# Kernel optimization log

Hardware: AMD Instinct MI355X
Metric: run time of the kernel (lower is better)

The kernel has to match this reference:

```python
import jax, jax.numpy as jnp
import numpy as np

B, N, K, D, H = 32, 4096, 8, 256, 512
ITERS = 3
LN_EPS = 1e-5  # torch LayerNorm default; self.eps is unused in forward


def _ln(x, g, b):
    m = jnp.mean(x, axis=-1, keepdims=True)
    v = jnp.mean(jnp.square(x - m), axis=-1, keepdims=True)
    return (x - m) * jax.lax.rsqrt(v + LN_EPS) * g + b


def setup_inputs() -> dict:
    key = jax.random.key(0)
    ks = jax.random.split(key, 16)
    s = 0.02
    return {
        "inputs": jax.random.normal(ks[0], (B, N, D), jnp.float32),
        "slots_init": jax.random.normal(ks[1], (B, K, D), jnp.float32),
        "ln_in_g": jnp.ones((D,), jnp.float32), "ln_in_b": jnp.zeros((D,), jnp.float32),
        "ln_s_g": jnp.ones((D,), jnp.float32), "ln_s_b": jnp.zeros((D,), jnp.float32),
        "ln_ff_g": jnp.ones((D,), jnp.float32), "ln_ff_b": jnp.zeros((D,), jnp.float32),
        "Wk": s * jax.random.normal(ks[2], (D, D), jnp.float32), "bk": jnp.zeros((D,), jnp.float32),
        "Wq": s * jax.random.normal(ks[3], (D, D), jnp.float32), "bq": jnp.zeros((D,), jnp.float32),
        "Wv": s * jax.random.normal(ks[4], (D, D), jnp.float32), "bv": jnp.zeros((D,), jnp.float32),
        "W_ih": s * jax.random.normal(ks[5], (3 * D, D), jnp.float32),
        "b_ih": jnp.zeros((3 * D,), jnp.float32),
        "W_hh": s * jax.random.normal(ks[6], (3 * D, D), jnp.float32),
        "b_hh": jnp.zeros((3 * D,), jnp.float32),
        "W1": s * jax.random.normal(ks[7], (H, D), jnp.float32), "b1": jnp.zeros((H,), jnp.float32),
        "W2": s * jax.random.normal(ks[8], (D, H), jnp.float32), "b2": jnp.zeros((D,), jnp.float32),
    }


def _gru_cell(x, h, W_ih, b_ih, W_hh, b_hh):
    # PyTorch GRUCell: gates in order r, z, n
    gi = x @ W_ih.T + b_ih  # [*, 3D]
    gh = h @ W_hh.T + b_hh
    ir, iz, inn = jnp.split(gi, 3, axis=-1)
    hr, hz, hn = jnp.split(gh, 3, axis=-1)
    r = jax.nn.sigmoid(ir + hr)
    z = jax.nn.sigmoid(iz + hz)
    n = jnp.tanh(inn + r * hn)
    return (1.0 - z) * n + z * h


def reference(inputs, slots_init, ln_in_g, ln_in_b, ln_s_g, ln_s_b, ln_ff_g, ln_ff_b,
              Wk, bk, Wq, bq, Wv, bv, W_ih, b_ih, W_hh, b_hh, W1, b1, W2, b2):
    d = inputs.shape[-1]
    x = _ln(inputs, ln_in_g, ln_in_b)  # [B,N,D]
    # k, v depend only on x; hoisted out of the loop (same math as source)
    k = x @ Wk.T + bk                  # project_inputs
    v = x @ Wv.T + bv                  # project_v
    scale = 1.0 / jnp.sqrt(jnp.asarray(d, inputs.dtype))
    slots = slots_init
    for _ in range(ITERS):
        slots_prev = slots
        q = _ln(slots, ln_s_g, ln_s_b) @ Wq.T + bq          # [B,K,D]
        attn_logits = jnp.einsum('bkd,bnd->bkn', q, k) * scale
        # competitive softmax over the SLOT axis (dim=1), not keys
        attn = jax.nn.softmax(attn_logits, axis=1)          # [B,K,N]
        updates = jnp.einsum('bkn,bnd->bkd', attn, v)
        slots = _gru_cell(updates, slots_prev, W_ih, b_ih, W_hh, b_hh)
        hdd = jax.nn.relu(_ln(slots, ln_ff_g, ln_ff_b) @ W1.T + b1)
        slots = slots + hdd @ W2.T + b2
    return slots
```

## Files before the change

### kernel.cpp

```cpp
#include <hip/hip_runtime.h>
#include <hip/hip_bf16.h>
#include <cstddef>
#include <cstdint>

#define BB 32
#define NN 4096
#define KK 8
#define DD 256
#define HH 512
#define LN_EPS 1e-5f
#define SCALE 0.0625f
#define NCHUNK 32

__device__ __forceinline__ float wave_sum(float v) {
#pragma unroll
  for (int off = 32; off >= 1; off >>= 1) v += __shfl_xor(v, off);
  return v;
}

__device__ __forceinline__ float sigmoidf_(float x) { return 1.0f / (1.0f + __expf(-x)); }

__device__ __forceinline__ float bflo(uint u) { return __uint_as_float(u << 16); }
__device__ __forceinline__ float bfhi(uint u) { return __uint_as_float(u & 0xffff0000u); }

#define OFF_G   0
#define OFF_W1  393216
#define OFF_W2  524288
#define OFF_WV  655360
#define OFF_WQ  720896
#define OFF_WK  786432
#define WB_ELEMS 851968

#define G_PRE (BB * KK)
#define G_W2B (512 * 11)
#define G_SETUP (G_PRE + G_W2B + 1)

__device__ __forceinline__ float dotp4(uint2 w, float4 s) {
  return __uint_as_float(w.x << 16) * s.x + __uint_as_float(w.x & 0xffff0000u) * s.y +
         __uint_as_float(w.y << 16) * s.z + __uint_as_float(w.y & 0xffff0000u) * s.w;
}

template <int OUT, int KL>
__device__ __forceinline__ float gemv_p(const ushort* __restrict__ wt, int j, int kb,
                                        const float* __restrict__ src) {
  const uint2* p = (const uint2*)(wt + ((size_t)(kb >> 2) * OUT + j) * 4);
  float a = 0.0f;
#pragma unroll 16
  for (int e = 0; e < KL / 4; ++e) {
    uint2 w = p[(size_t)e * OUT];
    float4 s = *(const float4*)(src + kb + e * 4);
    a += dotp4(w, s);
  }
  return a;
}

__global__ __launch_bounds__(256) void k_setup(
    const float* __restrict__ Wih, const float* __restrict__ Whh,
    const float* __restrict__ W1, const float* __restrict__ W2,
    const float* __restrict__ Wv, const float* __restrict__ Wq,
    const float* __restrict__ Wk, ushort* __restrict__ wb,
    const float* __restrict__ slots, const float* __restrict__ gs, const float* __restrict__ bs,
    const float* __restrict__ bq, const float* __restrict__ bk,
    const float* __restrict__ gi, const float* __restrict__ bi,
    const float* __restrict__ bv, float* __restrict__ bvw,
    float* __restrict__ qk, float* __restrict__ qb) {
  int blk = blockIdx.x;
  if (blk < G_PRE) {
    int row = blk;
    int t = threadIdx.x;
    int wid = t >> 6, lane = t & 63;
    __shared__ float lns[DD];
    __shared__ float qs[DD];
    __shared__ float rb[8];
    float sv = slots[(size_t)row * DD + t];
    float s = wave_sum(sv);
    float s2 = wave_sum(sv * sv);
    if (lane == 0) { rb[wid] = s; rb[4 + wid] = s2; }
    __syncthreads();
    float tot = rb[0] + rb[1] + rb[2] + rb[3];
    float tot2 = rb[4] + rb[5] + rb[6] + rb[7];
    float m = tot * (1.0f / DD);
    float var = tot2 * (1.0f / DD) - m * m;
    float rs = rsqrtf(var + LN_EPS);
    lns[t] = (sv - m) * rs * gs[t] + bs[t];
    __syncthreads();
    float acc = 0.0f;
    const float4* wr = (const float4*)(Wq + (size_t)t * DD);
#pragma unroll 4
    for (int e4 = 0; e4 < DD / 4; ++e4) {
      float4 w = wr[e4];
      float4 l = ((const float4*)lns)[e4];
      acc += w.x * l.x + w.y * l.y + w.z * l.z + w.w * l.w;
    }
    qs[t] = acc + bq[t];
    __syncthreads();
    float a2 = 0.0f;
    for (int d = 0; d < DD; ++d) a2 = fmaf(qs[d], Wk[(size_t)d * DD + t], a2);
    float a2S = SCALE * a2;
    qk[(size_t)row * DD + t] = a2S * gi[t];
    float pb = wave_sum(qs[t] * bk[t]);
    float pb2 = wave_sum(a2S * bi[t]);
    __syncthreads();
    if (lane == 0) { rb[wid] = pb; rb[4 + wid] = pb2; }
    __syncthreads();
    if (t == 0) qb[row] = SCALE * (rb[0] + rb[1] + rb[2] + rb[3]) + rb[4] + rb[5] + rb[6] + rb[7];
  } else if (blk < G_PRE + G_W2B) {
    int q2 = blk - G_PRE;
    int m = q2 >> 9;
    int idx = (q2 & 511) * 256 + threadIdx.x;
    const int sizes[11] = {65536, 65536, 65536, 65536, 65536, 65536, 131072, 131072, 65536, 65536, 65536};
    const int offs[11] = {OFF_G, OFF_G + 65536, OFF_G + 131072, OFF_G + 196608, OFF_G + 262144,
                          OFF_G + 327680, OFF_W1, OFF_W2, OFF_WV, OFF_WQ, OFF_WK};
    if (idx >= sizes[m]) return;
    int K = (m == 7) ? 512 : 256;
    int OUT = (m == 6) ? 512 : 256;
    int k = idx % K, j = idx / K;
    float v;
    switch (m) {
      case 0: case 1: case 2: v = Wih[((size_t)(m * 256 + j)) * 256 + k]; break;
      case 3: case 4: case 5: v = Whh[((size_t)((m - 3) * 256 + j)) * 256 + k]; break;
      case 6: v = W1[(size_t)j * 256 + k]; break;
      case 7: v = W2[(size_t)j * 512 + k]; break;
      case 8: v = Wv[(size_t)j * 256 + k] * gi[k]; break;
      case 9: v = Wq[(size_t)j * 256 + k]; break;
      default: v = Wk[(size_t)k * 256 + j]; break;
    }
    __hip_bfloat16 h = __float2bfloat16(v);
    wb[(size_t)offs[m] + (size_t)(k >> 2) * OUT * 4 + j * 4 + (k & 3)] = *(ushort*)&h;
  } else {
    int t = threadIdx.x;
    float a = bv[t];
    const float4* wr = (const float4*)(Wv + (size_t)t * DD);
    const float4* bb = (const float4*)bi;
#pragma unroll 4
    for (int e4 = 0; e4 < DD / 4; ++e4) {
      float4 w = wr[e4];
      float4 x = bb[e4];
      a += w.x * x.x + w.y * x.y + w.z * x.z + w.w * x.w;
    }
    bvw[t] = a;
  }
}

template <int DO_LN>
__global__ __launch_bounds__(256) void k_attn_t(const ushort* __restrict__ xb_in,
                                                ushort* __restrict__ xb_out,
                                                const float* __restrict__ inp,
                                                const float* __restrict__ qk,
                                                const float* __restrict__ qb,
                                                float* __restrict__ uxp,
                                                float* __restrict__ sap) {
  __shared__ __align__(16) float q_s[KK][DD];
  __shared__ __align__(16) ushort xt[4][32 * DD];
  __shared__ __align__(16) float a_s[4][KK][32];
  __shared__ float sred[4][KK];

  int t = threadIdx.x, wid = t >> 6, lane = t & 63;
  int bI = blockIdx.x >> 5, c = blockIdx.x & 31;
  int row0 = c * 128 + wid * 32;
  ushort* xw = xt[wid];

#pragma unroll
  for (int s = 0; s < KK; ++s) q_s[s][t] = qk[(size_t)bI * (KK * DD) + s * DD + t];
  float qbv[KK];
#pragma unroll
  for (int s = 0; s < KK; ++s) qbv[s] = qb[bI * KK + s];
  __syncthreads();

  int r = lane & 31, h = lane >> 5;

  if (DO_LN) {
    int q8 = lane & 7, lr = lane >> 3;
    const float* rp0 = inp + ((size_t)bI * NN + row0 + lr) * DD + q8 * 4;
    float4 cur[8];
#pragma unroll
    for (int i = 0; i < 8; ++i) cur[i] = *(const float4*)(rp0 + i * 32);
    for (int p = 0; p < 4; ++p) {
      float4 nxt[8];
      if (p < 3) {
#pragma unroll
        for (int i = 0; i < 8; ++i) nxt[i] = *(const float4*)(rp0 + (size_t)(p + 1) * 8 * DD + i * 32);
      }
      float s1 = 0.0f, s2 = 0.0f;
#pragma unroll
      for (int i = 0; i < 8; ++i) {
        s1 += cur[i].x + cur[i].y + cur[i].z + cur[i].w;
        s2 += cur[i].x * cur[i].x + cur[i].y * cur[i].y + cur[i].z * cur[i].z + cur[i].w * cur[i].w;
      }
      s1 += __shfl_xor(s1, 1); s2 += __shfl_xor(s2, 1);
      s1 += __shfl_xor(s1, 2); s2 += __shfl_xor(s2, 2);
      s1 += __shfl_xor(s1, 4); s2 += __shfl_xor(s2, 4);
      float m = s1 * (1.0f / DD);
      float var = s2 * (1.0f / DD) - m * m;
      float rs = rsqrtf(var + LN_EPS);
      int rr = p * 8 + lr;
      int hb = (q8 & 1) * 4;
#pragma unroll
      for (int i = 0; i < 8; ++i) {
        float y0 = (cur[i].x - m) * rs, y1 = (cur[i].y - m) * rs;
        float y2 = (cur[i].z - m) * rs, y3 = (cur[i].w - m) * rs;
        __hip_bfloat16 h0 = __float2bfloat16(y0), h1 = __float2bfloat16(y1);
        __hip_bfloat16 h2 = __float2bfloat16(y2), h3 = __float2bfloat16(y3);
        uint2 wv;
        wv.x = (uint)*(ushort*)&h0 | ((uint)*(ushort*)&h1 << 16);
        wv.y = (uint)*(ushort*)&h2 | ((uint)*(ushort*)&h3 << 16);
        int chunk = i * 4 + (q8 >> 1);
        *(uint2*)&xw[rr * DD + ((chunk ^ rr) << 3) + hb] = wv;
      }
      if (p < 3) {
#pragma unroll
        for (int i = 0; i < 8; ++i) cur[i] = nxt[i];
      }
    }
    ushort* xbt = xb_out + ((size_t)bI * NN + row0) * DD;
#pragma unroll
    for (int i = 0; i < 16; ++i) {
      uint4 v = *(const uint4*)&xw[i * 512 + lane * 8];
      *(uint4*)&xbt[i * 512 + lane * 8] = v;
    }
  } else {
    const ushort* srcb = xb_in + ((size_t)bI * NN + row0) * DD;
#pragma unroll
    for (int i = 0; i < 16; ++i) {
      __builtin_amdgcn_global_load_lds(
          (__attribute__((address_space(1))) void*)(srcb + i * 512 + lane * 8),
          (__attribute__((address_space(3))) void*)&xw[i * 512], 16, 0, 0);
    }
    asm volatile("s_waitcnt vmcnt(0)" ::: "memory");
  }

  float lg[KK] = {};
#pragma unroll 2
  for (int m = 0; m < 16; ++m) {
    int ch = m | (h << 4);
    uint4 xv = *(const uint4*)&xw[r * DD + ((ch ^ r) << 3)];
    float x0 = bflo(xv.x), x1 = bfhi(xv.x), x2 = bflo(xv.y), x3 = bfhi(xv.y);
    float x4 = bflo(xv.z), x5 = bfhi(xv.z), x6 = bflo(xv.w), x7 = bfhi(xv.w);
#pragma unroll
    for (int s = 0; s < KK; ++s) {
      const float* qp = &q_s[s][ch << 3];
      float4 qa = *(const float4*)qp;
      float4 qc = *(const float4*)(qp + 4);
      lg[s] += x0 * qa.x + x1 * qa.y + x2 * qa.z + x3 * qa.w +
               x4 * qc.x + x5 * qc.y + x6 * qc.z + x7 * qc.w;
    }
  }
#pragma unroll
  for (int s = 0; s < KK; ++s) lg[s] = lg[s] + __shfl_xor(lg[s], 32) + qbv[s];
  float mx = lg[0];
#pragma unroll
  for (int s = 1; s < KK; ++s) mx = fmaxf(mx, lg[s]);
  float a8[KK];
  float ssum = 0.0f;
#pragma unroll
  for (int s = 0; s < KK; ++s) { a8[s] = __expf(lg[s] - mx); ssum += a8[s]; }
  float rinv = __frcp_rn(ssum);
  if (h == 0) {
#pragma unroll
    for (int s = 0; s < KK; ++s) a_s[wid][s][r] = a8[s] * rinv;
  }

  int s8 = lane >> 3, j = lane & 7, rot = j >> 1;
  int kc[4];
#pragma unroll
  for (int cc = 0; cc < 4; ++cc) kc[cc] = 4 * j + ((cc + rot) & 3);
  float acc[4][8] = {};
  float sav = 0.0f;
  for (int r4 = 0; r4 < 8; ++r4) {
    float4 a4 = *(const float4*)&a_s[wid][s8][r4 * 4];
#pragma unroll
    for (int rr = 0; rr < 4; ++rr) {
      int r2 = r4 * 4 + rr;
      float av = (rr == 0) ? a4.x : (rr == 1) ? a4.y : (rr == 2) ? a4.z : a4.w;
      sav += av;
#pragma unroll
      for (int cc = 0; cc < 4; ++cc) {
        uint4 xv = *(const uint4*)&xw[r2 * DD + ((kc[cc] ^ r2) << 3)];
        acc[cc][0] = fmaf(av, bflo(xv.x), acc[cc][0]);
        acc[cc][1] = fmaf(av, bfhi(xv.x), acc[cc][1]);
        acc[cc][2] = fmaf(av, bflo(xv.y), acc[cc][2]);
        acc[cc][3] = fmaf(av, bfhi(xv.y), acc[cc][3]);
        acc[cc][4] = fmaf(av, bflo(xv.z), acc[cc][4]);
        acc[cc][5] = fmaf(av, bfhi(xv.z), acc[cc][5]);
        acc[cc][6] = fmaf(av, bflo(xv.w), acc[cc][6]);
        acc[cc][7] = fmaf(av, bfhi(xv.w), acc[cc][7]);
      }
    }
  }
  float* uxw = (float*)xw;
#pragma unroll
  for (int cc = 0; cc < 4; ++cc) {
    float4 v0 = make_float4(acc[cc][0], acc[cc][1], acc[cc][2], acc[cc][3]);
    float4 v1 = make_float4(acc[cc][4], acc[cc][5], acc[cc][6], acc[cc][7]);
    *(float4*)&uxw[s8 * DD + kc[cc] * 8] = v0;
    *(float4*)&uxw[s8 * DD + kc[cc] * 8 + 4] = v1;
  }
  if (j == 0) sred[wid][s8] = sav;
  __syncthreads();

  const float* x0f = (const float*)xt[0];
  const float* x1f = (const float*)xt[1];
  const float* x2f = (const float*)xt[2];
  const float* x3f = (const float*)xt[3];
  size_t obase = ((size_t)(bI * NCHUNK + c)) * (KK * DD);
#pragma unroll
  for (int u = 0; u < 8; ++u) {
    int idx = u * 256 + t;
    uxp[obase + idx] = x0f[idx] + x1f[idx] + x2f[idx] + x3f[idx];
  }
  if (t < 8)
    sap[((size_t)(bI * NCHUNK + c)) * KK + t] =
        sred[0][t] + sred[1][t] + sred[2][t] + sred[3][t];
}

__global__ __launch_bounds__(1024) void k_fused(const float* __restrict__ slots_in,
                                                const float* __restrict__ uxp,
                                                const float* __restrict__ sap,
                                                const ushort* __restrict__ wb,
                                                const float* __restrict__ bv,
                                                const float* __restrict__ bih, const float* __restrict__ bhh,
                                                const float* __restrict__ gff, const float* __restrict__ bff,
                                                const float* __restrict__ b1, const float* __restrict__ b2,
                                                const float* __restrict__ gs, const float* __restrict__ bs,
                                                const float* __restrict__ bq, const float* __restrict__ bk,
                                                const float* __restrict__ gi, const float* __restrict__ bi,
                                                float* __restrict__ dst,
                                                float* __restrict__ qk_out,
                                                float* __restrict__ qb_out,
                                                int last) {
  const ushort* WG = wb + OFF_G;
  const ushort* W1p = wb + OFF_W1;
  const ushort* W2p = wb + OFF_W2;
  const ushort* WVp = wb + OFF_WV;
  const ushort* WQp = wb + OFF_WQ;
  const ushort* WKp = wb + OFF_WK;

  __shared__ float ux_s[DD], h_s[DD], upd_s[DD], hn_s[DD], ln_s[DD];
  __shared__ float g_s[6][DD];
  __shared__ float hdd_s[HH];
  __shared__ float tmp4_s[4][DD];
  __shared__ float red_s[16];
  __shared__ float sA_s;
  float* tmpH = &tmp4_s[0][0];

  int t = threadIdx.x, d = t & 255, qr = t >> 8;
  int wid = t >> 6, lane = t & 63;
  int r = blockIdx.x, b = r >> 3, k = r & 7;

  {
    const float* p = uxp + (((size_t)(b * NCHUNK + qr * 8)) * KK + k) * DD + d;
    float s = 0.0f;
#pragma unroll
    for (int i = 0; i < 8; ++i) s += p[(size_t)i * KK * DD];
    tmp4_s[qr][d] = s;
  }
  if (t < 256) h_s[t] = slots_in[(size_t)r * DD + t];
  if (t >= 960) {
    int c = t - 960;
    float v = (c < NCHUNK) ? sap[((size_t)(b * NCHUNK + c)) * KK + k] : 0.0f;
    v = wave_sum(v);
    if (lane == 0) sA_s = v;
  }
  __syncthreads();
  if (t < 256) ux_s[t] = tmp4_s[0][t] + tmp4_s[1][t] + tmp4_s[2][t] + tmp4_s[3][t];
  __syncthreads();

  tmp4_s[qr][d] = gemv_p<256, 64>(WVp, d, qr * 64, ux_s);
  __syncthreads();
  if (t < 256) upd_s[t] = tmp4_s[0][t] + tmp4_s[1][t] + tmp4_s[2][t] + tmp4_s[3][t] + bv[t] * sA_s;
  __syncthreads();

  {
    int g = qr;
    const float* src = (g < 3) ? upd_s : h_s;
    float a = gemv_p<256, 256>(WG + (size_t)g * 65536, d, 0, src);
    g_s[g][d] = a + ((g < 3) ? bih[g * 256 + d] : bhh[d]);
    if (t < 512) {
      int g2 = 4 + (t >> 8), j2 = t & 255;
      float a2 = gemv_p<256, 256>(WG + (size_t)g2 * 65536, j2, 0, h_s);
      g_s[g2][j2] = a2 + bhh[(g2 - 3) * 256 + j2];
    }
  }
  __syncthreads();
  if (t < 256) {
    float rr = sigmoidf_(g_s[0][t] + g_s[3][t]);
    float zz = sigmoidf_(g_s[1][t] + g_s[4][t]);
    float nn = tanhf(g_s[2][t] + rr * g_s[5][t]);
    hn_s[t] = (1.0f - zz) * nn + zz * h_s[t];
  }
  __syncthreads();

  if (t < 256) {
    float v = hn_s[t];
    float sm = wave_sum(v), sq = wave_sum(v * v);
    if (lane == 0) { red_s[wid] = sm; red_s[8 + wid] = sq; }
  }
  __syncthreads();
  if (t < 256) {
    float v = hn_s[t];
    float tot = red_s[0] + red_s[1] + red_s[2] + red_s[3];
    float tot2 = red_s[8] + red_s[9] + red_s[10] + red_s[11];
    float m = tot * (1.0f / DD);
    float var = tot2 * (1.0f / DD) - m * m;
    float rs = rsqrtf(var + LN_EPS);
    ln_s[t] = (v - m) * rs * gff[t] + bff[t];
  }
  __syncthreads();

  {
    int o = t & 511, kh = t >> 9;
    tmpH[kh * 512 + o] = gemv_p<512, 128>(W1p, o, kh * 128, ln_s);
  }
  __syncthreads();
  if (t < 512) hdd_s[t] = fmaxf(tmpH[t] + tmpH[512 + t] + b1[t], 0.0f);
  __syncthreads();

  tmp4_s[qr][d] = gemv_p<256, 128>(W2p, d, qr * 128, hdd_s);
  __syncthreads();
  if (t < 256) {
    float o = hn_s[t] + tmp4_s[0][t] + tmp4_s[1][t] + tmp4_s[2][t] + tmp4_s[3][t] + b2[t];
    dst[(size_t)r * DD + t] = o;
    ux_s[t] = o;
  }
  __syncthreads();

  if (!last) {
    if (t < 256) {
      float v = ux_s[t];
      float sm = wave_sum(v), sq = wave_sum(v * v);
      if (lane == 0) { red_s[wid] = sm; red_s[8 + wid] = sq; }
    }
    __syncthreads();
    if (t < 256) {
      float v = ux_s[t];
      float tot = red_s[0] + red_s[1] + red_s[2] + red_s[3];
      float tot2 = red_s[8] + red_s[9] + red_s[10] + red_s[11];
      float m = tot * (1.0f / DD);
      float var = tot2 * (1.0f / DD) - m * m;
      float rs = rsqrtf(var + LN_EPS);
      ln_s[t] = (v - m) * rs * gs[t] + bs[t];
    }
    __syncthreads();
    tmp4_s[qr][d] = gemv_p<256, 64>(WQp, d, qr * 64, ln_s);
    __syncthreads();
    if (t < 256) {
      float qv = tmp4_s[0][t] + tmp4_s[1][t] + tmp4_s[2][t] + tmp4_s[3][t] + bq[t];
      upd_s[t] = qv;
      float sb = wave_sum(qv * bk[t]);
      if (lane == 0) red_s[wid] = sb;
    }
    __syncthreads();
    {
      float a = gemv_p<256, 64>(WKp, d, qr * 64, upd_s);
      tmp4_s[qr][d] = a;
    }
    __syncthreads();
    if (t < 256) {
      float qkv = SCALE * (tmp4_s[0][t] + tmp4_s[1][t] + tmp4_s[2][t] + tmp4_s[3][t]);
      qk_out[(size_t)r * DD + t] = qkv * gi[t];
      float pb2 = wave_sum(qkv * bi[t]);
      if (lane == 0) red_s[8 + wid] = pb2;
    }
    __syncthreads();
    if (t == 0) qb_out[r] = SCALE * (red_s[0] + red_s[1] + red_s[2] + red_s[3]) +
                            red_s[8] + red_s[9] + red_s[10] + red_s[11];
  }
}

extern "C" void kernel_launch(void* const* d_in, const int* in_sizes, int n_in,
                              void* d_out, int out_size, void* d_ws, size_t ws_size,
                              hipStream_t stream) {
  const float* inputs = (const float*)d_in[0];
  const float* slots_init = (const float*)d_in[1];
  const float* ln_in_g = (const float*)d_in[2];
  const float* ln_in_b = (const float*)d_in[3];
  const float* ln_s_g = (const float*)d_in[4];
  const float* ln_s_b = (const float*)d_in[5];
  const float* ln_ff_g = (const float*)d_in[6];
  const float* ln_ff_b = (const float*)d_in[7];
  const float* Wk = (const float*)d_in[8];
  const float* bk = (const float*)d_in[9];
  const float* Wq = (const float*)d_in[10];
  const float* bq = (const float*)d_in[11];
  const float* Wv = (const float*)d_in[12];
  const float* bv = (const float*)d_in[13];
  const float* Wih = (const float*)d_in[14];
  const float* bih = (const float*)d_in[15];
  const float* Whh = (const float*)d_in[16];
  const float* bhh = (const float*)d_in[17];
  const float* W1 = (const float*)d_in[18];
  const float* b1 = (const float*)d_in[19];
  const float* W2 = (const float*)d_in[20];
  const float* b2 = (const float*)d_in[21];
  float* outp = (float*)d_out;

  char* w = (char*)d_ws;
  ushort* xb = (ushort*)w;       w += (size_t)BB * NN * DD * 2;
  float* qk = (float*)w;         w += (size_t)BB * KK * DD * 4;
  float* qb = (float*)w;         w += (size_t)BB * KK * 4;
  float* uxp = (float*)w;        w += (size_t)BB * NCHUNK * KK * DD * 4;
  float* sap = (float*)w;        w += (size_t)BB * NCHUNK * KK * 4;
  float* slots_ws = (float*)w;   w += (size_t)BB * KK * DD * 4;
  ushort* wb = (ushort*)w;       w += (size_t)WB_ELEMS * 2;
  float* bvw = (float*)w;        w += (size_t)DD * 4;

  k_setup<<<G_SETUP, 256, 0, stream>>>(Wih, Whh, W1, W2, Wv, Wq, Wk, wb,
                                       slots_init, ln_s_g, ln_s_b, bq, bk,
                                       ln_in_g, ln_in_b, bv, bvw, qk, qb);

  for (int it = 0; it < 3; ++it) {
    if (it == 0)
      k_attn_t<1><<<BB * NCHUNK, 256, 0, stream>>>(nullptr, xb, inputs, qk, qb, uxp, sap);
    else
      k_attn_t<0><<<BB * NCHUNK, 256, 0, stream>>>(xb, nullptr, nullptr, qk, qb, uxp, sap);
    const float* sin = (it == 0) ? slots_init : slots_ws;
    float* dst = (it == 2) ? outp : slots_ws;
    k_fused<<<BB * KK, 1024, 0, stream>>>(sin, uxp, sap, wb,
                                          bvw, bih, bhh, ln_ff_g, ln_ff_b, b1, b2,
                                          ln_s_g, ln_s_b, bq, bk, ln_in_g, ln_in_b,
                                          dst, qk, qb, (it == 2) ? 1 : 0);
  }
}
```

Before: 264.7 us.

## Compute attention logits and updates with bf16 MFMA using hi/lo split operands

```diff
diff --git a/kernel.cpp b/kernel.cpp
--- a/kernel.cpp
+++ b/kernel.cpp
@@ -19,9 +19,6 @@
 }
 
 __device__ __forceinline__ float sigmoidf_(float x) { return 1.0f / (1.0f + __expf(-x)); }
-
-__device__ __forceinline__ float bflo(uint u) { return __uint_as_float(u << 16); }
-__device__ __forceinline__ float bfhi(uint u) { return __uint_as_float(u & 0xffff0000u); }
 
 #define OFF_G   0
 #define OFF_W1  393216
@@ -150,24 +147,37 @@
                                                 const float* __restrict__ qb,
                                                 float* __restrict__ uxp,
                                                 float* __restrict__ sap) {
-  __shared__ __align__(16) float q_s[KK][DD];
-  __shared__ __align__(16) ushort xt[4][32 * DD];
-  __shared__ __align__(16) float a_s[4][KK][32];
-  __shared__ float sred[4][KK];
+  typedef __attribute__((ext_vector_type(8))) short short8;
+  typedef __attribute__((ext_vector_type(4))) float f32x4;
+
+  __shared__ __align__(16) ushort q_l[16 * 256];
+  __shared__ __align__(16) ushort xt[4][32 * 256];
 
   int t = threadIdx.x, wid = t >> 6, lane = t & 63;
   int bI = blockIdx.x >> 5, c = blockIdx.x & 31;
+  int lm = lane & 15, g = lane >> 4;
+  ushort* xw = xt[wid];
+
+  {
+    const float* qkb = qk + (size_t)bI * (KK * DD);
+#pragma unroll
+    for (int s = 0; s < 16; ++s) {
+      float qv = qkb[(s & 7) * 256 + t];
+      __hip_bfloat16 hb = __float2bfloat16(qv);
+      ushort st = *(ushort*)&hb;
+      if (s >= 8) {
+        float lo = qv - __bfloat162float(hb);
+        __hip_bfloat16 lb2 = __float2bfloat16(lo);
+        st = *(ushort*)&lb2;
+      }
+      int pos = (t >> 3) ^ (s & 7);
+      q_l[s * 256 + pos * 8 + (t & 7)] = st;
+    }
+  }
+  float qbv = qb[bI * 8 + (lane & 7)];
+  __syncthreads();
+
   int row0 = c * 128 + wid * 32;
-  ushort* xw = xt[wid];
-
-#pragma unroll
-  for (int s = 0; s < KK; ++s) q_s[s][t] = qk[(size_t)bI * (KK * DD) + s * DD + t];
-  float qbv[KK];
-#pragma unroll
-  for (int s = 0; s < KK; ++s) qbv[s] = qb[bI * KK + s];
-  __syncthreads();
-
-  int r = lane & 31, h = lane >> 5;
 
   if (DO_LN) {
     int q8 = lane & 7, lr = lane >> 3;
@@ -194,7 +204,7 @@
       float var = s2 * (1.0f / DD) - m * m;
       float rs = rsqrtf(var + LN_EPS);
       int rr = p * 8 + lr;
-      int hb = (q8 & 1) * 4;
+      int hb2 = (q8 & 1) * 4;
 #pragma unroll
       for (int i = 0; i < 8; ++i) {
         float y0 = (cur[i].x - m) * rs, y1 = (cur[i].y - m) * rs;
@@ -205,7 +215,7 @@
         wv.x = (uint)*(ushort*)&h0 | ((uint)*(ushort*)&h1 << 16);
         wv.y = (uint)*(ushort*)&h2 | ((uint)*(ushort*)&h3 << 16);
         int chunk = i * 4 + (q8 >> 1);
-        *(uint2*)&xw[rr * DD + ((chunk ^ rr) << 3) + hb] = wv;
+        *(uint2*)&xw[rr * DD + ((chunk ^ rr) << 3) + hb2] = wv;
       }
       if (p < 3) {
 #pragma unroll
@@ -227,90 +237,125 @@
           (__attribute__((address_space(3))) void*)&xw[i * 512], 16, 0, 0);
     }
     asm volatile("s_waitcnt vmcnt(0)" ::: "memory");
-  }
-
-  float lg[KK] = {};
-#pragma unroll 2
-  for (int m = 0; m < 16; ++m) {
-    int ch = m | (h << 4);
-    uint4 xv = *(const uint4*)&xw[r * DD + ((ch ^ r) << 3)];
-    float x0 = bflo(xv.x), x1 = bfhi(xv.x), x2 = bflo(xv.y), x3 = bfhi(xv.y);
-    float x4 = bflo(xv.z), x5 = bfhi(xv.z), x6 = bflo(xv.w), x7 = bfhi(xv.w);
-#pragma unroll
-    for (int s = 0; s < KK; ++s) {
-      const float* qp = &q_s[s][ch << 3];
-      float4 qa = *(const float4*)qp;
-      float4 qc = *(const float4*)(qp + 4);
-      lg[s] += x0 * qa.x + x1 * qa.y + x2 * qa.z + x3 * qa.w +
-               x4 * qc.x + x5 * qc.y + x6 * qc.z + x7 * qc.w;
-    }
-  }
-#pragma unroll
-  for (int s = 0; s < KK; ++s) lg[s] = lg[s] + __shfl_xor(lg[s], 32) + qbv[s];
-  float mx = lg[0];
-#pragma unroll
-  for (int s = 1; s < KK; ++s) mx = fmaxf(mx, lg[s]);
-  float a8[KK];
-  float ssum = 0.0f;
-#pragma unroll
-  for (int s = 0; s < KK; ++s) { a8[s] = __expf(lg[s] - mx); ssum += a8[s]; }
-  float rinv = __frcp_rn(ssum);
-  if (h == 0) {
-#pragma unroll
-    for (int s = 0; s < KK; ++s) a_s[wid][s][r] = a8[s] * rinv;
-  }
-
-  int s8 = lane >> 3, j = lane & 7, rot = j >> 1;
-  int kc[4];
-#pragma unroll
-  for (int cc = 0; cc < 4; ++cc) kc[cc] = 4 * j + ((cc + rot) & 3);
-  float acc[4][8] = {};
-  float sav = 0.0f;
-  for (int r4 = 0; r4 < 8; ++r4) {
-    float4 a4 = *(const float4*)&a_s[wid][s8][r4 * 4];
-#pragma unroll
-    for (int rr = 0; rr < 4; ++rr) {
-      int r2 = r4 * 4 + rr;
-      float av = (rr == 0) ? a4.x : (rr == 1) ? a4.y : (rr == 2) ? a4.z : a4.w;
-      sav += av;
-#pragma unroll
-      for (int cc = 0; cc < 4; ++cc) {
-        uint4 xv = *(const uint4*)&xw[r2 * DD + ((kc[cc] ^ r2) << 3)];
-        acc[cc][0] = fmaf(av, bflo(xv.x), acc[cc][0]);
-        acc[cc][1] = fmaf(av, bfhi(xv.x), acc[cc][1]);
-        acc[cc][2] = fmaf(av, bflo(xv.y), acc[cc][2]);
-        acc[cc][3] = fmaf(av, bfhi(xv.y), acc[cc][3]);
-        acc[cc][4] = fmaf(av, bflo(xv.z), acc[cc][4]);
-        acc[cc][5] = fmaf(av, bfhi(xv.z), acc[cc][5]);
-        acc[cc][6] = fmaf(av, bflo(xv.w), acc[cc][6]);
-        acc[cc][7] = fmaf(av, bfhi(xv.w), acc[cc][7]);
-      }
-    }
-  }
-  float* uxw = (float*)xw;
-#pragma unroll
-  for (int cc = 0; cc < 4; ++cc) {
-    float4 v0 = make_float4(acc[cc][0], acc[cc][1], acc[cc][2], acc[cc][3]);
-    float4 v1 = make_float4(acc[cc][4], acc[cc][5], acc[cc][6], acc[cc][7]);
-    *(float4*)&uxw[s8 * DD + kc[cc] * 8] = v0;
-    *(float4*)&uxw[s8 * DD + kc[cc] * 8 + 4] = v1;
-  }
-  if (j == 0) sred[wid][s8] = sav;
-  __syncthreads();
-
-  const float* x0f = (const float*)xt[0];
-  const float* x1f = (const float*)xt[1];
-  const float* x2f = (const float*)xt[2];
-  const float* x3f = (const float*)xt[3];
-  size_t obase = ((size_t)(bI * NCHUNK + c)) * (KK * DD);
-#pragma unroll
-  for (int u = 0; u < 8; ++u) {
-    int idx = u * 256 + t;
-    uxp[obase + idx] = x0f[idx] + x1f[idx] + x2f[idx] + x3f[idx];
-  }
-  if (t < 8)
-    sap[((size_t)(bI * NCHUNK + c)) * KK + t] =
-        sred[0][t] + sred[1][t] + sred[2][t] + sred[3][t];
+    __builtin_amdgcn_sched_barrier(0);
+  }
+
+  union V16 { uint4 u; short8 s; };
+  int rA = lm, rB = lm + 16;
+  f32x4 ac0 = {}, ac1 = {};
+#pragma unroll
+  for (int kk = 0; kk < 8; ++kk) {
+    V16 qf, x0, x1;
+    int ch = kk * 4 + g;
+    qf.u = *(const uint4*)&q_l[lm * 256 + ((ch ^ (lm & 7)) << 3)];
+    x0.u = *(const uint4*)&xw[rA * 256 + ((ch ^ rA) << 3)];
+    x1.u = *(const uint4*)&xw[rB * 256 + ((ch ^ rB) << 3)];
+    ac0 = __builtin_amdgcn_mfma_f32_16x16x32_bf16(x0.s, qf.s, ac0, 0, 0, 0);
+    ac1 = __builtin_amdgcn_mfma_f32_16x16x32_bf16(x1.s, qf.s, ac1, 0, 0, 0);
+  }
+
+  float a0[4], a1[4];
+  {
+    float lv0[4], lv1[4], mx0[4], mx1[4], ss0[4], ss1[4];
+#pragma unroll
+    for (int r = 0; r < 4; ++r) {
+      lv0[r] = ac0[r] + __shfl_xor(ac0[r], 8) + qbv;
+      lv1[r] = ac1[r] + __shfl_xor(ac1[r], 8) + qbv;
+      mx0[r] = lv0[r]; mx1[r] = lv1[r];
+    }
+#pragma unroll
+    for (int off = 1; off <= 4; off <<= 1) {
+#pragma unroll
+      for (int r = 0; r < 4; ++r) {
+        mx0[r] = fmaxf(mx0[r], __shfl_xor(mx0[r], off));
+        mx1[r] = fmaxf(mx1[r], __shfl_xor(mx1[r], off));
+      }
+    }
+#pragma unroll
+    for (int r = 0; r < 4; ++r) {
+      a0[r] = __expf(lv0[r] - mx0[r]);
+      a1[r] = __expf(lv1[r] - mx1[r]);
+      ss0[r] = a0[r]; ss1[r] = a1[r];
+    }
+#pragma unroll
+    for (int off = 1; off <= 4; off <<= 1) {
+#pragma unroll
+      for (int r = 0; r < 4; ++r) {
+        ss0[r] += __shfl_xor(ss0[r], off);
+        ss1[r] += __shfl_xor(ss1[r], off);
+      }
+    }
+#pragma unroll
+    for (int r = 0; r < 4; ++r) {
+      a0[r] *= __frcp_rn(ss0[r]);
+      a1[r] *= __frcp_rn(ss1[r]);
+    }
+  }
+  float sacc = 0.0f;
+#pragma unroll
+  for (int r = 0; r < 4; ++r) sacc += a0[r] + a1[r];
+  sacc += __shfl_xor(sacc, 16);
+  sacc += __shfl_xor(sacc, 32);
+
+  union A2u { ushort us[8]; short8 s; } au;
+  bool lop = (lane & 8) != 0;
+#pragma unroll
+  for (int e = 0; e < 8; ++e) {
+    float av = (e < 4) ? a0[e] : a1[e - 4];
+    __hip_bfloat16 hb = __float2bfloat16(av);
+    if (lop) {
+      float lo = av - __bfloat162float(hb);
+      hb = __float2bfloat16(lo);
+    }
+    au.us[e] = *(ushort*)&hb;
+  }
+
+  f32x4 av4[16];
+#pragma unroll
+  for (int i = 0; i < 16; ++i) av4[i] = (f32x4){0.0f, 0.0f, 0.0f, 0.0f};
+#pragma unroll
+  for (int dc = 0; dc < 16; ++dc) {
+    int d = dc * 16 + lm, dch = d >> 3, d7 = d & 7;
+    union A2u bu;
+#pragma unroll
+    for (int e = 0; e < 4; ++e) {
+      int r1 = 4 * g + e;
+      int r2 = 16 + 4 * g + e;
+      bu.us[e] = xw[r1 * 256 + ((dch ^ r1) << 3) + d7];
+      bu.us[4 + e] = xw[r2 * 256 + ((dch ^ r2) << 3) + d7];
+    }
+    av4[dc] = __builtin_amdgcn_mfma_f32_16x16x32_bf16(au.s, bu.s, av4[dc], 0, 0, 0);
+  }
+
+  float* uxwf = (float*)xw;
+#pragma unroll
+  for (int dc = 0; dc < 16; ++dc) {
+#pragma unroll
+    for (int r = 0; r < 4; ++r) {
+      float v = av4[dc][r];
+      float o = v + __shfl_xor(v, 32);
+      if (lane < 32) uxwf[(g * 4 + r) * 256 + dc * 16 + lm] = o;
+    }
+  }
+  __syncthreads();
+  float* sredf = (float*)q_l;
+  if (lane < 8) sredf[wid * 8 + lane] = sacc;
+  __syncthreads();
+  {
+    const float* x0f = (const float*)xt[0];
+    const float* x1f = (const float*)xt[1];
+    const float* x2f = (const float*)xt[2];
+    const float* x3f = (const float*)xt[3];
+    size_t obase = ((size_t)(bI * NCHUNK + c)) * (KK * DD);
+#pragma unroll
+    for (int u = 0; u < 8; ++u) {
+      int idx = u * 256 + t;
+      uxp[obase + idx] = x0f[idx] + x1f[idx] + x2f[idx] + x3f[idx];
+    }
+    if (t < 8)
+      sap[((size_t)(bI * NCHUNK + c)) * KK + t] =
+          sredf[t] + sredf[8 + t] + sredf[16 + t] + sredf[24 + t];
+  }
 }
 
 __global__ __launch_bounds__(1024) void k_fused(const float* __restrict__ slots_in,
```

Measured after the change: 232.7 us. 12.1% less time.
